# Kernel optimization log

Measured on AMD Instinct MI355X. Metric: run time of the kernel, lower is better.

Reference implementation:

```python
import jax, jax.numpy as jnp
import numpy as np
from jax.scipy.linalg import lu_factor, lu_solve

DT = 0.1          # dt
EPS = 0.01        # epsilon
STEPS = 40        # max sweep iterations
TOL = 1e-4        # convergence tolerance


def setup_inputs() -> dict:
    key = jax.random.key(0)
    ks = jax.random.split(key, 9)
    B, D_IN, U, D_OUT = 2048, 1024, 1024, 1000
    def lin(kw, kb, out_f, in_f):
        bound = 1.0 / np.sqrt(in_f)
        W = jax.random.uniform(kw, (out_f, in_f), jnp.float32, -bound, bound)
        b = jax.random.uniform(kb, (out_f,), jnp.float32, -bound, bound)
        return W, b
    x = jax.random.normal(ks[0], (B, D_IN), jnp.float32)
    W_in, b_in = lin(ks[1], ks[2], U, D_IN)
    W1, b1 = lin(ks[3], ks[4], U, U)
    W2, b2 = lin(ks[5], ks[6], U, U)
    W_out, b_out = lin(ks[7], ks[8], D_OUT, U)
    return {"x": x, "W_in": W_in, "b_in": b_in, "W1": W1, "b1": b1,
            "W2": W2, "b2": b2, "W_out": W_out, "b_out": b_out}


def _make_A(W):
    # A = [[I, dt*W], [-dt*W^T, (1+dt/eps)*I]], shape [2u, 2u]
    u = W.shape[0]
    I = jnp.eye(u, dtype=W.dtype)
    return jnp.block([[I, DT * W], [-DT * W.T, (1.0 + DT / EPS) * I]])


def _run_sweep(z_in, rhs1, rhs2, A1, A2):
    # Gauss-Seidel-like sweeping: z1 = A1^{-1}(rhs1+z_in); z2 = A2^{-1}(rhs2+z1)
    # A is identical across the batch, so factor once and solve for all rhs.
    lu1 = lu_factor(A1)
    lu2 = lu_factor(A2)
    r1 = rhs1 + z_in  # constant across sweeps
    def cond(c):
        _, _, err, step = c
        return (step < STEPS) & (err > TOL)
    def body(c):
        z1, z2, _, step = c
        y1 = lu_solve(lu1, r1.T).T
        e1 = jnp.mean(jnp.linalg.norm(z1 - y1, axis=1))
        y2 = lu_solve(lu2, (rhs2 + y1).T).T
        e2 = jnp.mean(jnp.linalg.norm(z2 - y2, axis=1))
        return y1, y2, 0.5 * (e1 + e2), step + 1
    z1, z2, _, _ = jax.lax.while_loop(
        cond, body, (z_in, z_in, jnp.float32(10.0), jnp.int32(0)))
    return z1, z2


@jax.custom_vjp
def _hook(z, A):
    # Forward identity; backward replaces grad g with A^{-T} g (per-row),
    # mirroring the torch register_hook(torch.solve(grad, J^T)).
    return z

def _hook_fwd(z, A):
    return z, A

def _hook_bwd(A, g):
    gz = jnp.linalg.solve(A.T, g.T).T
    return gz, jnp.zeros_like(A)

_hook.defvjp(_hook_fwd, _hook_bwd)


def _implicit(z_in_blk, z_l, W, b, A):
    u = W.shape[0]
    u_in, v_in = z_in_blk[:, :u], z_in_blk[:, u:]
    u_out = u_in + DT * b - DT * (z_l[:, u:] @ W.T)
    v_out = v_in + DT * (z_l[:, :u] @ W) - (DT / EPS) * (z_l[:, u:] - jnp.tanh(u_in))
    z = jnp.concatenate([u_out, v_out], axis=1)
    return _hook(z, jax.lax.stop_gradient(A))


def reference(x, W_in, b_in, W1, b1, W2, b2, W_out, b_out):
    sg = jax.lax.stop_gradient
    u = W1.shape[0]
    B = x.shape[0]
    h = x @ W_in.T + b_in                       # [B, u]
    z_in = jnp.concatenate([h, jnp.tanh(h)], axis=1)  # [B, 2u]
    A1 = _make_A(W1)
    A2 = _make_A(W2)
    # relax rhs = [dt*b, dt/eps * tanh(u_in)] (built from z_in for both blocks)
    tz = (DT / EPS) * jnp.tanh(z_in[:, :u])
    rhs1 = jnp.concatenate([jnp.broadcast_to(DT * b1, (B, u)), tz], axis=1)
    rhs2 = jnp.concatenate([jnp.broadcast_to(DT * b2, (B, u)), tz], axis=1)
    # sweep loop runs under no_grad in the original -> stop_gradient everywhere
    z1, z2 = _run_sweep(sg(z_in), sg(rhs1), sg(rhs2), sg(A1), sg(A2))
    z = _implicit(z_in, z1, W1, b1, A1)
    z = _implicit(z, z2, W2, b2, A2)
    logits = z[:, :u] @ W_out.T + b_out
    return jax.nn.softmax(logits, axis=1)
```

## Files before the change

kernel.cpp:

```cpp
#include <hip/hip_runtime.h>


typedef short bf16x8 __attribute__((ext_vector_type(8)));
typedef float f32x4 __attribute__((ext_vector_type(4)));

#define M1 1048576

__device__ __forceinline__ unsigned short f2b(float f) {
  union { float f; unsigned int u; } v; v.f = f;
  unsigned int u = v.u;
  return (unsigned short)((u + 0x7FFFu + ((u >> 16) & 1u)) >> 16);
}

__device__ __forceinline__ void gload16(const void* g, void* l) {
  __builtin_amdgcn_global_load_lds(
      (const __attribute__((address_space(1))) unsigned int*)g,
      (__attribute__((address_space(3))) unsigned int*)l, 16, 0, 0);
}

template <int MODE, int NKT>
__device__ __forceinline__ void gemm64(
    const unsigned short* __restrict__ A, int lda,
    const unsigned short* __restrict__ B, int ldb,
    int bx, int by,
    const float* bias0, const float* bias1, const float* src0,
    float* dstf0, float* dstf1,
    unsigned short* dstbf, int ldc, unsigned short* dstbf2,
    short (*As)[4096], short (*Bs)[4096]) {
  const int tid = threadIdx.x;
  const int lane = tid & 63;
  const int wid = tid >> 6;
  const int wr = wid >> 1;
  const int wc = wid & 1;
  const int m0 = bx * 64;
  const int n0 = by * 64;
  const int l15 = lane & 15;
  const int kb = lane >> 4;

  const int sr = tid >> 3;
  const int sg = ((tid & 7) - sr) & 7;
  const unsigned short* Asrc = A + (size_t)(m0 + sr) * lda + sg * 8;
  const unsigned short* Bsrc = B + (size_t)(n0 + sr) * ldb + sg * 8;
  const size_t a32 = (size_t)32 * lda;
  const size_t b32 = (size_t)32 * ldb;
  const int o0 = tid * 8;
  const int o1 = 2048 + tid * 8;

  f32x4 acc[2][2];
#pragma unroll
  for (int f = 0; f < 2; ++f)
#pragma unroll
    for (int g = 0; g < 2; ++g) acc[f][g] = (f32x4){0.f, 0.f, 0.f, 0.f};

#define STG(kt, buf)                                  \
  do {                                                \
    gload16(Asrc + (kt) * 64, &As[(buf)][o0]);        \
    gload16(Asrc + a32 + (kt) * 64, &As[(buf)][o1]);  \
    gload16(Bsrc + (kt) * 64, &Bs[(buf)][o0]);        \
    gload16(Bsrc + b32 + (kt) * 64, &Bs[(buf)][o1]);  \
  } while (0)

  STG(0, 0);
  STG(1, 1);

#pragma unroll
  for (int t = 0; t < NKT; ++t) {
    if (t < NKT - 1) {
      asm volatile("s_waitcnt vmcnt(4)" ::: "memory");
    } else {
      asm volatile("s_waitcnt vmcnt(0)" ::: "memory");
    }
    __builtin_amdgcn_sched_barrier(0);
    __builtin_amdgcn_s_barrier();
    __builtin_amdgcn_sched_barrier(0);
    if (t + 2 < NKT) STG(t + 2, (t + 2) % 3);
    const int cb = t % 3;
    bf16x8 av[2][2], bv[2][2];
#pragma unroll
    for (int f = 0; f < 2; ++f) {
      const int ra = wr * 32 + f * 16 + l15;
#pragma unroll
      for (int ks = 0; ks < 2; ++ks) {
        const int qa = (ks * 4 + kb + l15) & 7;
        av[f][ks] = *reinterpret_cast<const bf16x8*>(&As[cb][ra * 64 + qa * 8]);
      }
    }
#pragma unroll
    for (int g = 0; g < 2; ++g) {
      const int rb = wc * 32 + g * 16 + l15;
#pragma unroll
      for (int ks = 0; ks < 2; ++ks) {
        const int qb2 = (ks * 4 + kb + l15) & 7;
        bv[g][ks] = *reinterpret_cast<const bf16x8*>(&Bs[cb][rb * 64 + qb2 * 8]);
      }
    }
#pragma unroll
    for (int ks = 0; ks < 2; ++ks)
#pragma unroll
      for (int f = 0; f < 2; ++f)
#pragma unroll
        for (int g = 0; g < 2; ++g)
          acc[f][g] = __builtin_amdgcn_mfma_f32_16x16x32_bf16(av[f][ks], bv[g][ks], acc[f][g], 0, 0, 0);
  }
#undef STG

#pragma unroll
  for (int f = 0; f < 2; ++f) {
#pragma unroll
    for (int g = 0; g < 2; ++g) {
#pragma unroll
      for (int j = 0; j < 4; ++j) {
        int m = m0 + wr * 32 + f * 16 + kb * 4 + j;
        int n = n0 + wc * 32 + g * 16 + l15;
        size_t fidx = (size_t)m * 1024 + n;
        size_t cidx = (size_t)m * ldc + n;
        float v = acc[f][g][j];
        if (MODE == 0) {
          dstbf[cidx] = f2b(v);
        } else if (MODE == 1) {
          float h = v + bias0[n];
          float thv = tanhf(h);
          float r = h + 0.1f * bias1[n];
          dstf0[fidx] = r;
          dstf1[fidx] = thv;
          dstbf[cidx] = f2b(r);
        } else if (MODE == 2) {
          dstbf[cidx] = f2b(11.0f * src0[fidx] + 0.1f * v);
        } else if (MODE == 4) {
          float r = src0[fidx] + 0.1f * bias0[n] - 0.1f * v;
          dstf0[fidx] = r;
          dstbf[cidx] = f2b(0.1f * r);
        } else if (MODE == 5) {
          dstbf[cidx] = f2b(10.0f * src0[fidx] + v);
        } else if (MODE == 7) {
          dstbf[cidx] = f2b(src0[fidx] - 0.1f * v);
        } else if (MODE == 8) {
          dstf0[fidx] = v + bias0[n];
        } else {
          float q = (m == n ? (1.0f / 11.0f) : 0.0f) - (0.01f / 121.0f) * v;
          unsigned short qq = f2b(q);
          dstbf[cidx] = qq;
          if (dstbf2) dstbf2[(size_t)m * 2048 + n] = qq;
        }
      }
    }
  }
}

__device__ __forceinline__ void map512(int b, int& bx, int& by) {
  bx = ((b & 7) << 2) | ((b >> 3) & 3);
  by = b >> 5;
}
__device__ __forceinline__ void map256(int r, int& bx, int& by) {
  bx = ((r & 7) << 1) | ((r >> 3) & 1);
  by = (r >> 4) & 15;
}

__global__ __launch_bounds__(256) void k_D2(
    const unsigned short* __restrict__ xb, const unsigned short* __restrict__ winb,
    const unsigned short* __restrict__ wtb,
    const float* __restrict__ b_in, const float* __restrict__ b1,
    float* __restrict__ r1u, float* __restrict__ th,
    unsigned short* __restrict__ zb0, unsigned short* __restrict__ qb,
    unsigned short* __restrict__ bcat) {
  __shared__ short As[3][4096];
  __shared__ short Bs[3][4096];
  const int b = blockIdx.x;
  int bx, by;
  if (b < 512) {
    map512(b, bx, by);
    gemm64<1, 16>(xb, 1024, winb, 1024, bx, by, b_in, b1, nullptr,
                  r1u, th, zb0, 1024, nullptr, As, Bs);
  } else {
    int r = b - 512;
    const int z = r >> 8;
    map256(r & 255, bx, by);
    const unsigned short* wt = wtb + (size_t)z * M1;
    gemm64<9, 16>(wt, 1024, wt, 1024, bx, by, nullptr, nullptr, nullptr,
                  nullptr, nullptr, qb + (size_t)z * M1, 1024,
                  z == 0 ? bcat : nullptr, As, Bs);
  }
}

__global__ __launch_bounds__(256) void k_D3(
    const unsigned short* __restrict__ wb, const unsigned short* __restrict__ qb,
    const unsigned short* __restrict__ zb0, const unsigned short* __restrict__ wtb,
    const float* __restrict__ th,
    unsigned short* __restrict__ a1b, unsigned short* __restrict__ a2b,
    unsigned short* __restrict__ zcat) {
  __shared__ short As[3][4096];
  __shared__ short Bs[3][4096];
  const int b = blockIdx.x;
  int bx, by;
  if (b < 512) {
    const int z = b >> 8;
    map256(b & 255, bx, by);
    gemm64<0, 16>(wb + (size_t)z * M1, 1024, qb + (size_t)z * M1, 1024, bx, by,
                  nullptr, nullptr, nullptr, nullptr, nullptr,
                  z == 0 ? a1b : a2b, 1024, nullptr, As, Bs);
  } else {
    map512(b - 512, bx, by);
    gemm64<2, 16>(zb0, 1024, wtb, 1024, bx, by, nullptr, nullptr, th,
                  nullptr, nullptr, zcat, 2048, nullptr, As, Bs);
  }
}

__global__ __launch_bounds__(256) void k_D4(
    const unsigned short* __restrict__ zcat, const unsigned short* __restrict__ a1b,
    const float* __restrict__ b2, const float* __restrict__ r1u,
    float* __restrict__ r2u, unsigned short* __restrict__ zcat_hi) {
  __shared__ short As[3][4096];
  __shared__ short Bs[3][4096];
  int bx, by;
  map512(blockIdx.x, bx, by);
  gemm64<4, 16>(zcat, 2048, a1b, 1024, bx, by, b2, nullptr, r1u,
                r2u, nullptr, zcat_hi, 2048, nullptr, As, Bs);
}

__global__ __launch_bounds__(256) void k_D5(
    const unsigned short* __restrict__ zcat, const unsigned short* __restrict__ bcat,
    const float* __restrict__ th, unsigned short* __restrict__ zb2) {
  __shared__ short As[3][4096];
  __shared__ short Bs[3][4096];
  int bx, by;
  map512(blockIdx.x, bx, by);
  gemm64<5, 32>(zcat, 2048, bcat, 2048, bx, by, nullptr, nullptr, th,
                nullptr, nullptr, zb2, 1024, nullptr, As, Bs);
}

__global__ __launch_bounds__(256) void k_D6(
    const unsigned short* __restrict__ zb2, const unsigned short* __restrict__ a2b,
    const float* __restrict__ r2u, unsigned short* __restrict__ zb3) {
  __shared__ short As[3][4096];
  __shared__ short Bs[3][4096];
  int bx, by;
  map512(blockIdx.x, bx, by);
  gemm64<7, 16>(zb2, 1024, a2b, 1024, bx, by, nullptr, nullptr, r2u,
                nullptr, nullptr, zb3, 1024, nullptr, As, Bs);
}

__global__ __launch_bounds__(256) void k_D7(
    const unsigned short* __restrict__ zb3, const unsigned short* __restrict__ woutb,
    const float* __restrict__ boutp, float* __restrict__ lgts) {
  __shared__ short As[3][4096];
  __shared__ short Bs[3][4096];
  int bx, by;
  map512(blockIdx.x, bx, by);
  gemm64<8, 16>(zb3, 1024, woutb, 1024, bx, by, boutp, nullptr, nullptr,
                lgts, nullptr, nullptr, 1024, nullptr, As, Bs);
}

__global__ __launch_bounds__(256) void k_prep(
    const float* __restrict__ x, const float* __restrict__ Win,
    const float* __restrict__ W1, const float* __restrict__ W2,
    const float* __restrict__ Wout, const float* __restrict__ bout,
    unsigned short* __restrict__ xb, unsigned short* __restrict__ winb,
    unsigned short* __restrict__ wb, unsigned short* __restrict__ wtb,
    unsigned short* __restrict__ woutb, float* __restrict__ boutp,
    unsigned short* __restrict__ bcat) {
  __shared__ float tile[32][33];
  const int b = blockIdx.x;
  const int tid = threadIdx.x;
  if (b < 2048) {
    const int isW2 = (b >> 10) & 1;
    const float* W = isW2 ? W2 : W1;
    unsigned short* Wb = wb + ((size_t)isW2 << 20);
    unsigned short* WTb = wtb + ((size_t)isW2 << 20);
    const int rem = b & 1023;
    const int tbx = rem & 31, tby = rem >> 5;
    const int tx = tid & 31, ty = tid >> 5;
#pragma unroll
    for (int i = ty; i < 32; i += 8) {
      float v = W[(size_t)(tby * 32 + i) * 1024 + tbx * 32 + tx];
      tile[i][tx] = v;
      Wb[(size_t)(tby * 32 + i) * 1024 + tbx * 32 + tx] = f2b(v);
    }
    __syncthreads();
#pragma unroll
    for (int i = ty; i < 32; i += 8) {
      unsigned short t2 = f2b(tile[tx][i]);
      int rr = tbx * 32 + i, cc = tby * 32 + tx;
      WTb[(size_t)rr * 1024 + cc] = t2;
      if (isW2) bcat[(size_t)rr * 2048 + 1024 + cc] = t2;
    }
  } else if (b < 4096) {
    int i = (b - 2048) * 256 + tid;
    float4 v = ((const float4*)x)[i];
    ((ushort4*)xb)[i] = (ushort4){f2b(v.x), f2b(v.y), f2b(v.z), f2b(v.w)};
  } else if (b < 5120) {
    int i = (b - 4096) * 256 + tid;
    float4 v = ((const float4*)Win)[i];
    ((ushort4*)winb)[i] = (ushort4){f2b(v.x), f2b(v.y), f2b(v.z), f2b(v.w)};
  } else if (b < 6144) {
    int i = (b - 5120) * 256 + tid;
    ushort4 o = (ushort4){0, 0, 0, 0};
    if ((i >> 8) < 1000) {
      float4 v = ((const float4*)Wout)[i];
      o = (ushort4){f2b(v.x), f2b(v.y), f2b(v.z), f2b(v.w)};
    }
    ((ushort4*)woutb)[i] = o;
  } else {
    for (int j = tid; j < 1024; j += 256) boutp[j] = (j < 1000) ? bout[j] : 0.0f;
  }
}

__global__ __launch_bounds__(256) void k_softmax(const float* __restrict__ lg,
                                                 float* __restrict__ out) {
  const int r = blockIdx.x;
  const float* p = lg + (size_t)r * 1024;
  float* q = out + (size_t)r * 1000;
  const int tid = threadIdx.x;
  const int lane = tid & 63;
  const int w = tid >> 6;
  __shared__ float redm[4];
  __shared__ float reds[4];
  float m = -3.0e38f;
  for (int i = tid; i < 1000; i += 256) m = fmaxf(m, p[i]);
#pragma unroll
  for (int o = 32; o > 0; o >>= 1) m = fmaxf(m, __shfl_xor(m, o));
  if (lane == 0) redm[w] = m;
  __syncthreads();
  m = fmaxf(fmaxf(redm[0], redm[1]), fmaxf(redm[2], redm[3]));
  float s = 0.0f;
  for (int i = tid; i < 1000; i += 256) {
    float e = __expf(p[i] - m);
    q[i] = e;
    s += e;
  }
#pragma unroll
  for (int o = 32; o > 0; o >>= 1) s += __shfl_xor(s, o);
  if (lane == 0) reds[w] = s;
  __syncthreads();
  float inv = 1.0f / (reds[0] + reds[1] + reds[2] + reds[3]);
  for (int i = tid; i < 1000; i += 256) q[i] *= inv;
}

extern "C" void kernel_launch(void* const* d_in, const int* in_sizes, int n_in,
                              void* d_out, int out_size, void* d_ws, size_t ws_size,
                              hipStream_t stream) {
  const float* x = (const float*)d_in[0];
  const float* W_in = (const float*)d_in[1];
  const float* b_in = (const float*)d_in[2];
  const float* W1 = (const float*)d_in[3];
  const float* b1 = (const float*)d_in[4];
  const float* W2 = (const float*)d_in[5];
  const float* b2 = (const float*)d_in[6];
  const float* W_out = (const float*)d_in[7];
  const float* b_out = (const float*)d_in[8];
  float* out = (float*)d_out;

  const size_t Bm = 2048, U = 1024;
  char* ws = (char*)d_ws;
  size_t off = 0;
  auto alloc = [&](size_t bytes) -> void* {
    void* p = ws + off;
    off += (bytes + 255) & ~(size_t)255;
    return p;
  };
  unsigned short* xb = (unsigned short*)alloc(Bm * U * 2);
  unsigned short* winb = (unsigned short*)alloc((size_t)M1 * 2);
  unsigned short* wb = (unsigned short*)alloc(2 * (size_t)M1 * 2);
  unsigned short* wtb = (unsigned short*)alloc(2 * (size_t)M1 * 2);
  unsigned short* qb = (unsigned short*)alloc(2 * (size_t)M1 * 2);
  unsigned short* a1b = (unsigned short*)alloc((size_t)M1 * 2);
  unsigned short* a2b = (unsigned short*)alloc((size_t)M1 * 2);
  unsigned short* bcat = (unsigned short*)alloc(2 * (size_t)M1 * 2);
  unsigned short* woutb = (unsigned short*)alloc((size_t)M1 * 2);
  float* boutp = (float*)alloc(U * 4);
  unsigned short* zb0 = (unsigned short*)alloc(Bm * U * 2);
  unsigned short* zcat = (unsigned short*)alloc(Bm * 2 * U * 2);
  unsigned short* zb2 = (unsigned short*)alloc(Bm * U * 2);
  unsigned short* zb3 = (unsigned short*)alloc(Bm * U * 2);
  float* r1u = (float*)alloc(Bm * U * 4);
  float* th = (float*)alloc(Bm * U * 4);
  float* r2u = (float*)alloc(Bm * U * 4);
  float* lgts = (float*)alloc(Bm * U * 4);

  k_prep<<<6145, 256, 0, stream>>>(x, W_in, W1, W2, W_out, b_out,
                                   xb, winb, wb, wtb, woutb, boutp, bcat);
  k_D2<<<1024, 256, 0, stream>>>(xb, winb, wtb, b_in, b1, r1u, th, zb0, qb, bcat);
  k_D3<<<1024, 256, 0, stream>>>(wb, qb, zb0, wtb, th, a1b, a2b, zcat);
  k_D4<<<512, 256, 0, stream>>>(zcat, a1b, b2, r1u, r2u, zcat + 1024);
  k_D5<<<512, 256, 0, stream>>>(zcat, bcat, th, zb2);
  k_D6<<<512, 256, 0, stream>>>(zb2, a2b, r2u, zb3);
  k_D7<<<512, 256, 0, stream>>>(zb3, woutb, boutp, lgts);
  k_softmax<<<2048, 256, 0, stream>>>(lgts, out);
}
```

Measured before the change: 111.5 us.

## Precompose weight products to collapse the sequential GEMM chain into fewer stages

Reassociates the closed-form solve chain so that weight-only products (W2·W1-derived matrices, the second-block inverse folded into the output projection, and a bias projection vector) are computed up front. Those products run in parallel with the activation GEMMs. This cuts the dependent batch-sized GEMM launches from six kernels to four and removes the intermediate fp32 activation buffers. In exchange it adds several 1024x1024 weight-side GEMMs and a naive per-row dot-product path, and it folds more bf16 rounding into the precomposed matrices, which may affect accuracy.

```diff
diff --git a/kernel.cpp b/kernel.cpp
--- a/kernel.cpp
+++ b/kernel.cpp
@@ -10,6 +10,9 @@
   union { float f; unsigned int u; } v; v.f = f;
   unsigned int u = v.u;
   return (unsigned short)((u + 0x7FFFu + ((u >> 16) & 1u)) >> 16);
+}
+__device__ __forceinline__ float b2f(unsigned short u) {
+  union { unsigned u; float f; } x; x.u = ((unsigned)u) << 16; return x.f;
 }
 
 __device__ __forceinline__ void gload16(const void* g, void* l) {
@@ -24,8 +27,9 @@
     const unsigned short* __restrict__ B, int ldb,
     int bx, int by,
     const float* bias0, const float* bias1, const float* src0,
+    const unsigned short* srcb,
     float* dstf0, float* dstf1,
-    unsigned short* dstbf, int ldc, unsigned short* dstbf2,
+    unsigned short* dstbf, int ldc,
     short (*As)[4096], short (*Bs)[4096]) {
   const int tid = threadIdx.x;
   const int lane = tid & 63;
@@ -126,21 +130,18 @@
           dstbf[cidx] = f2b(r);
         } else if (MODE == 2) {
           dstbf[cidx] = f2b(11.0f * src0[fidx] + 0.1f * v);
+        } else if (MODE == 3) {
+          dstbf[cidx] = f2b(b2f(srcb[fidx]) - 0.01f * v);
         } else if (MODE == 4) {
-          float r = src0[fidx] + 0.1f * bias0[n] - 0.1f * v;
-          dstf0[fidx] = r;
-          dstbf[cidx] = f2b(0.1f * r);
+          dstbf[cidx] = f2b(src0[fidx] + 0.1f * bias0[n] - 0.1f * v);
         } else if (MODE == 5) {
-          dstbf[cidx] = f2b(10.0f * src0[fidx] + v);
-        } else if (MODE == 7) {
-          dstbf[cidx] = f2b(src0[fidx] - 0.1f * v);
+          dstbf[cidx] = f2b(10.0f * src0[fidx] + bias1[n] + v);
+        } else if (MODE == 6) {
+          dstbf[cidx] = f2b(-0.1f * v);
         } else if (MODE == 8) {
           dstf0[fidx] = v + bias0[n];
         } else {
-          float q = (m == n ? (1.0f / 11.0f) : 0.0f) - (0.01f / 121.0f) * v;
-          unsigned short qq = f2b(q);
-          dstbf[cidx] = qq;
-          if (dstbf2) dstbf2[(size_t)m * 2048 + n] = qq;
+          dstbf[cidx] = f2b((m == n ? (1.0f / 11.0f) : 0.0f) - (0.01f / 121.0f) * v);
         }
       }
     }
@@ -156,98 +157,111 @@
   by = (r >> 4) & 15;
 }
 
-__global__ __launch_bounds__(256) void k_D2(
+__global__ __launch_bounds__(256) void k_P2(
     const unsigned short* __restrict__ xb, const unsigned short* __restrict__ winb,
-    const unsigned short* __restrict__ wtb,
+    const unsigned short* __restrict__ wtb1, const unsigned short* __restrict__ wtb2,
+    const unsigned short* __restrict__ bcat5,
     const float* __restrict__ b_in, const float* __restrict__ b1,
+    const float* __restrict__ b2,
     float* __restrict__ r1u, float* __restrict__ th,
-    unsigned short* __restrict__ zb0, unsigned short* __restrict__ qb,
-    unsigned short* __restrict__ bcat) {
+    unsigned short* __restrict__ acat4, unsigned short* __restrict__ qb1,
+    unsigned short* __restrict__ qb2, unsigned short* __restrict__ m12t,
+    unsigned short* __restrict__ h2buf, float* __restrict__ rcon) {
   __shared__ short As[3][4096];
   __shared__ short Bs[3][4096];
   const int b = blockIdx.x;
   int bx, by;
   if (b < 512) {
     map512(b, bx, by);
-    gemm64<1, 16>(xb, 1024, winb, 1024, bx, by, b_in, b1, nullptr,
-                  r1u, th, zb0, 1024, nullptr, As, Bs);
+    gemm64<1, 16>(xb, 1024, winb, 1024, bx, by, b_in, b1, nullptr, nullptr,
+                  r1u, th, acat4 + 1024, 2048, As, Bs);
+  } else if (b < 1024) {
+    const int z = (b - 512) >> 8;
+    map256((b - 512) & 255, bx, by);
+    const unsigned short* wt = z ? wtb2 : wtb1;
+    gemm64<9, 16>(wt, 1024, wt, 1024, bx, by, nullptr, nullptr, nullptr, nullptr,
+                  nullptr, nullptr, z ? qb2 : qb1, 1024, As, Bs);
+  } else if (b < 1280) {
+    map256(b - 1024, bx, by);
+    gemm64<0, 16>(wtb2, 1024, wtb1, 1024, bx, by, nullptr, nullptr, nullptr, nullptr,
+                  nullptr, nullptr, m12t, 1024, As, Bs);
+  } else if (b < 1536) {
+    map256(b - 1280, bx, by);
+    gemm64<0, 16>(bcat5, 2048, wtb2, 1024, bx, by, nullptr, nullptr, nullptr, nullptr,
+                  nullptr, nullptr, h2buf, 1024, As, Bs);
   } else {
-    int r = b - 512;
-    const int z = r >> 8;
-    map256(r & 255, bx, by);
-    const unsigned short* wt = wtb + (size_t)z * M1;
-    gemm64<9, 16>(wt, 1024, wt, 1024, bx, by, nullptr, nullptr, nullptr,
-                  nullptr, nullptr, qb + (size_t)z * M1, 1024,
-                  z == 0 ? bcat : nullptr, As, Bs);
-  }
-}
-
-__global__ __launch_bounds__(256) void k_D3(
-    const unsigned short* __restrict__ wb, const unsigned short* __restrict__ qb,
-    const unsigned short* __restrict__ zb0, const unsigned short* __restrict__ wtb,
-    const float* __restrict__ th,
-    unsigned short* __restrict__ a1b, unsigned short* __restrict__ a2b,
-    unsigned short* __restrict__ zcat) {
+    int n = (b - 1536) * 256 + threadIdx.x;
+    const unsigned short* row = wtb2 + (size_t)n * 1024;
+    float s = 0.f;
+    for (int k = 0; k < 1024; k += 4) {
+      ushort4 w4 = *reinterpret_cast<const ushort4*>(row + k);
+      s += b2[k] * b2f(w4.x) + b2[k + 1] * b2f(w4.y) +
+           b2[k + 2] * b2f(w4.z) + b2[k + 3] * b2f(w4.w);
+    }
+    rcon[n] = 0.01f * s;
+  }
+}
+
+__global__ __launch_bounds__(256) void k_P3(
+    const unsigned short* __restrict__ acat4, const unsigned short* __restrict__ wtb1,
+    const unsigned short* __restrict__ wb1, const unsigned short* __restrict__ qb1,
+    const unsigned short* __restrict__ qb2, const unsigned short* __restrict__ m12t,
+    const unsigned short* __restrict__ h2buf, const float* __restrict__ th,
+    unsigned short* __restrict__ acat4lo, unsigned short* __restrict__ a1b,
+    unsigned short* __restrict__ bcat4, unsigned short* __restrict__ bcat5hi) {
   __shared__ short As[3][4096];
   __shared__ short Bs[3][4096];
   const int b = blockIdx.x;
   int bx, by;
   if (b < 512) {
-    const int z = b >> 8;
-    map256(b & 255, bx, by);
-    gemm64<0, 16>(wb + (size_t)z * M1, 1024, qb + (size_t)z * M1, 1024, bx, by,
-                  nullptr, nullptr, nullptr, nullptr, nullptr,
-                  z == 0 ? a1b : a2b, 1024, nullptr, As, Bs);
+    map512(b, bx, by);
+    gemm64<2, 16>(acat4 + 1024, 2048, wtb1, 1024, bx, by, nullptr, nullptr, th,
+                  nullptr, nullptr, nullptr, acat4lo, 2048, As, Bs);
+  } else if (b < 768) {
+    map256(b - 512, bx, by);
+    gemm64<0, 16>(wb1, 1024, qb1, 1024, bx, by, nullptr, nullptr, nullptr, nullptr,
+                  nullptr, nullptr, a1b, 1024, As, Bs);
+  } else if (b < 1024) {
+    map256(b - 768, bx, by);
+    gemm64<3, 16>(m12t, 1024, qb1, 1024, bx, by, nullptr, nullptr, nullptr, qb1,
+                  nullptr, nullptr, bcat4, 2048, As, Bs);
+  } else {
+    map256(b - 1024, bx, by);
+    gemm64<6, 16>(h2buf, 1024, qb2, 1024, bx, by, nullptr, nullptr, nullptr, nullptr,
+                  nullptr, nullptr, bcat5hi, 2048, As, Bs);
+  }
+}
+
+__global__ __launch_bounds__(256) void k_P4(
+    const unsigned short* __restrict__ acat4, const unsigned short* __restrict__ a1b,
+    const unsigned short* __restrict__ bcat4,
+    const float* __restrict__ b2, const float* __restrict__ r1u,
+    const float* __restrict__ th, const float* __restrict__ rcon,
+    unsigned short* __restrict__ acat5) {
+  __shared__ short As[3][4096];
+  __shared__ short Bs[3][4096];
+  const int b = blockIdx.x;
+  int bx, by;
+  if (b < 512) {
+    map512(b, bx, by);
+    gemm64<4, 16>(acat4, 2048, a1b, 1024, bx, by, b2, nullptr, r1u, nullptr,
+                  nullptr, nullptr, acat5, 2048, As, Bs);
   } else {
     map512(b - 512, bx, by);
-    gemm64<2, 16>(zb0, 1024, wtb, 1024, bx, by, nullptr, nullptr, th,
-                  nullptr, nullptr, zcat, 2048, nullptr, As, Bs);
-  }
-}
-
-__global__ __launch_bounds__(256) void k_D4(
-    const unsigned short* __restrict__ zcat, const unsigned short* __restrict__ a1b,
-    const float* __restrict__ b2, const float* __restrict__ r1u,
-    float* __restrict__ r2u, unsigned short* __restrict__ zcat_hi) {
-  __shared__ short As[3][4096];
-  __shared__ short Bs[3][4096];
-  int bx, by;
-  map512(blockIdx.x, bx, by);
-  gemm64<4, 16>(zcat, 2048, a1b, 1024, bx, by, b2, nullptr, r1u,
-                r2u, nullptr, zcat_hi, 2048, nullptr, As, Bs);
-}
-
-__global__ __launch_bounds__(256) void k_D5(
-    const unsigned short* __restrict__ zcat, const unsigned short* __restrict__ bcat,
-    const float* __restrict__ th, unsigned short* __restrict__ zb2) {
-  __shared__ short As[3][4096];
-  __shared__ short Bs[3][4096];
-  int bx, by;
-  map512(blockIdx.x, bx, by);
-  gemm64<5, 32>(zcat, 2048, bcat, 2048, bx, by, nullptr, nullptr, th,
-                nullptr, nullptr, zb2, 1024, nullptr, As, Bs);
-}
-
-__global__ __launch_bounds__(256) void k_D6(
-    const unsigned short* __restrict__ zb2, const unsigned short* __restrict__ a2b,
-    const float* __restrict__ r2u, unsigned short* __restrict__ zb3) {
-  __shared__ short As[3][4096];
-  __shared__ short Bs[3][4096];
-  int bx, by;
-  map512(blockIdx.x, bx, by);
-  gemm64<7, 16>(zb2, 1024, a2b, 1024, bx, by, nullptr, nullptr, r2u,
-                nullptr, nullptr, zb3, 1024, nullptr, As, Bs);
-}
-
-__global__ __launch_bounds__(256) void k_D7(
-    const unsigned short* __restrict__ zb3, const unsigned short* __restrict__ woutb,
+    gemm64<5, 32>(acat4, 2048, bcat4, 2048, bx, by, nullptr, rcon, th, nullptr,
+                  nullptr, nullptr, acat5 + 1024, 2048, As, Bs);
+  }
+}
+
+__global__ __launch_bounds__(256) void k_P5(
+    const unsigned short* __restrict__ acat5, const unsigned short* __restrict__ bcat5,
     const float* __restrict__ boutp, float* __restrict__ lgts) {
   __shared__ short As[3][4096];
   __shared__ short Bs[3][4096];
   int bx, by;
   map512(blockIdx.x, bx, by);
-  gemm64<8, 16>(zb3, 1024, woutb, 1024, bx, by, boutp, nullptr, nullptr,
-                lgts, nullptr, nullptr, 1024, nullptr, As, Bs);
+  gemm64<8, 32>(acat5, 2048, bcat5, 2048, bx, by, boutp, nullptr, nullptr, nullptr,
+                lgts, nullptr, nullptr, 1024, As, Bs);
 }
 
 __global__ __launch_bounds__(256) void k_prep(
@@ -255,17 +269,15 @@
     const float* __restrict__ W1, const float* __restrict__ W2,
     const float* __restrict__ Wout, const float* __restrict__ bout,
     unsigned short* __restrict__ xb, unsigned short* __restrict__ winb,
-    unsigned short* __restrict__ wb, unsigned short* __restrict__ wtb,
-    unsigned short* __restrict__ woutb, float* __restrict__ boutp,
-    unsigned short* __restrict__ bcat) {
+    unsigned short* __restrict__ wb1, unsigned short* __restrict__ wtb1,
+    unsigned short* __restrict__ wtb2, unsigned short* __restrict__ bcat4,
+    unsigned short* __restrict__ bcat5, float* __restrict__ boutp) {
   __shared__ float tile[32][33];
   const int b = blockIdx.x;
   const int tid = threadIdx.x;
   if (b < 2048) {
     const int isW2 = (b >> 10) & 1;
     const float* W = isW2 ? W2 : W1;
-    unsigned short* Wb = wb + ((size_t)isW2 << 20);
-    unsigned short* WTb = wtb + ((size_t)isW2 << 20);
     const int rem = b & 1023;
     const int tbx = rem & 31, tby = rem >> 5;
     const int tx = tid & 31, ty = tid >> 5;
@@ -273,15 +285,19 @@
     for (int i = ty; i < 32; i += 8) {
       float v = W[(size_t)(tby * 32 + i) * 1024 + tbx * 32 + tx];
       tile[i][tx] = v;
-      Wb[(size_t)(tby * 32 + i) * 1024 + tbx * 32 + tx] = f2b(v);
+      if (!isW2) wb1[(size_t)(tby * 32 + i) * 1024 + tbx * 32 + tx] = f2b(v);
     }
     __syncthreads();
 #pragma unroll
     for (int i = ty; i < 32; i += 8) {
-      unsigned short t2 = f2b(tile[tx][i]);
+      float vt = tile[tx][i];
       int rr = tbx * 32 + i, cc = tby * 32 + tx;
-      WTb[(size_t)rr * 1024 + cc] = t2;
-      if (isW2) bcat[(size_t)rr * 2048 + 1024 + cc] = t2;
+      if (isW2) {
+        wtb2[(size_t)rr * 1024 + cc] = f2b(vt);
+        bcat4[(size_t)rr * 2048 + 1024 + cc] = f2b(0.1f * vt);
+      } else {
+        wtb1[(size_t)rr * 1024 + cc] = f2b(vt);
+      }
     }
   } else if (b < 4096) {
     int i = (b - 2048) * 256 + tid;
@@ -293,12 +309,13 @@
     ((ushort4*)winb)[i] = (ushort4){f2b(v.x), f2b(v.y), f2b(v.z), f2b(v.w)};
   } else if (b < 6144) {
     int i = (b - 5120) * 256 + tid;
+    int row = i >> 8, c4 = i & 255;
     ushort4 o = (ushort4){0, 0, 0, 0};
-    if ((i >> 8) < 1000) {
+    if (row < 1000) {
       float4 v = ((const float4*)Wout)[i];
       o = (ushort4){f2b(v.x), f2b(v.y), f2b(v.z), f2b(v.w)};
     }
-    ((ushort4*)woutb)[i] = o;
+    ((ushort4*)bcat5)[(size_t)row * 512 + c4] = o;
   } else {
     for (int j = tid; j < 1024; j += 256) boutp[j] = (j < 1000) ? bout[j] : 0.0f;
   }
@@ -359,30 +376,31 @@
   };
   unsigned short* xb = (unsigned short*)alloc(Bm * U * 2);
   unsigned short* winb = (unsigned short*)alloc((size_t)M1 * 2);
-  unsigned short* wb = (unsigned short*)alloc(2 * (size_t)M1 * 2);
-  unsigned short* wtb = (unsigned short*)alloc(2 * (size_t)M1 * 2);
-  unsigned short* qb = (unsigned short*)alloc(2 * (size_t)M1 * 2);
+  unsigned short* wb1 = (unsigned short*)alloc((size_t)M1 * 2);
+  unsigned short* wtb1 = (unsigned short*)alloc((size_t)M1 * 2);
+  unsigned short* wtb2 = (unsigned short*)alloc((size_t)M1 * 2);
+  unsigned short* qb1 = (unsigned short*)alloc((size_t)M1 * 2);
+  unsigned short* qb2 = (unsigned short*)alloc((size_t)M1 * 2);
+  unsigned short* m12t = (unsigned short*)alloc((size_t)M1 * 2);
+  unsigned short* h2buf = (unsigned short*)alloc((size_t)M1 * 2);
   unsigned short* a1b = (unsigned short*)alloc((size_t)M1 * 2);
-  unsigned short* a2b = (unsigned short*)alloc((size_t)M1 * 2);
-  unsigned short* bcat = (unsigned short*)alloc(2 * (size_t)M1 * 2);
-  unsigned short* woutb = (unsigned short*)alloc((size_t)M1 * 2);
+  unsigned short* acat4 = (unsigned short*)alloc(Bm * 2 * U * 2);
+  unsigned short* bcat4 = (unsigned short*)alloc(2 * (size_t)M1 * 2);
+  unsigned short* acat5 = (unsigned short*)alloc(Bm * 2 * U * 2);
+  unsigned short* bcat5 = (unsigned short*)alloc(2 * (size_t)M1 * 2);
   float* boutp = (float*)alloc(U * 4);
-  unsigned short* zb0 = (unsigned short*)alloc(Bm * U * 2);
-  unsigned short* zcat = (unsigned short*)alloc(Bm * 2 * U * 2);
-  unsigned short* zb2 = (unsigned short*)alloc(Bm * U * 2);
-  unsigned short* zb3 = (unsigned short*)alloc(Bm * U * 2);
+  float* rcon = (float*)alloc(U * 4);
   float* r1u = (float*)alloc(Bm * U * 4);
   float* th = (float*)alloc(Bm * U * 4);
-  float* r2u = (float*)alloc(Bm * U * 4);
   float* lgts = (float*)alloc(Bm * U * 4);
 
   k_prep<<<6145, 256, 0, stream>>>(x, W_in, W1, W2, W_out, b_out,
-                                   xb, winb, wb, wtb, woutb, boutp, bcat);
-  k_D2<<<1024, 256, 0, stream>>>(xb, winb, wtb, b_in, b1, r1u, th, zb0, qb, bcat);
-  k_D3<<<1024, 256, 0, stream>>>(wb, qb, zb0, wtb, th, a1b, a2b, zcat);
-  k_D4<<<512, 256, 0, stream>>>(zcat, a1b, b2, r1u, r2u, zcat + 1024);
-  k_D5<<<512, 256, 0, stream>>>(zcat, bcat, th, zb2);
-  k_D6<<<512, 256, 0, stream>>>(zb2, a2b, r2u, zb3);
-  k_D7<<<512, 256, 0, stream>>>(zb3, woutb, boutp, lgts);
+                                   xb, winb, wb1, wtb1, wtb2, bcat4, bcat5, boutp);
+  k_P2<<<1540, 256, 0, stream>>>(xb, winb, wtb1, wtb2, bcat5, b_in, b1, b2,
+                                 r1u, th, acat4, qb1, qb2, m12t, h2buf, rcon);
+  k_P3<<<1280, 256, 0, stream>>>(acat4, wtb1, wb1, qb1, qb2, m12t, h2buf, th,
+                                 acat4, a1b, bcat4, bcat5 + 1024);
+  k_P4<<<1024, 256, 0, stream>>>(acat4, a1b, bcat4, b2, r1u, th, rcon, acat5);
+  k_P5<<<512, 256, 0, stream>>>(acat5, bcat5, boutp, lgts);
   k_softmax<<<2048, 256, 0, stream>>>(lgts, out);
 }
```

New measurement: 123.0 us. +10.3%, slower.
